# Performance work log

Hardware: AMD Instinct MI355X
Metric: run time of the kernel (lower is better)

Reference implementation:

```python
import jax, jax.numpy as jnp
import numpy as np

EPS = 1e-5


def _gcn_norm(edge_index, N):
    # symmetric GCN normalization with self-loops: D^-1/2 (A+I) D^-1/2
    row, col = edge_index[0], edge_index[1]
    loop = jnp.arange(N, dtype=row.dtype)
    row_f = jnp.concatenate([row, loop])
    col_f = jnp.concatenate([col, loop])
    deg = jax.ops.segment_sum(jnp.ones_like(row_f, dtype=jnp.float32), row_f, num_segments=N)
    dinv = jnp.where(deg > 0, jax.lax.rsqrt(jnp.maximum(deg, 1.0)), 0.0)
    norm = dinv[row_f] * dinv[col_f]  # [E+N]
    return row_f, col_f, norm


def _gcn_conv(h, W, b, row_f, col_f, norm, N):
    h = h @ W  # [N, C_out] small GEMM
    msg = h[col_f] * norm[:, None]  # gather over edges  [E+N, C_out]
    return jax.ops.segment_sum(msg, row_f, num_segments=N) + b


def _bn_eval(h, gamma, beta, mean, var):
    return (h - mean) * jax.lax.rsqrt(var + EPS) * gamma + beta


def setup_inputs() -> dict:
    key = jax.random.key(0)
    ks = jax.random.split(key, 12)
    N, E = 100000, 1600000
    C_in, C_hid, C_out = 64, 64, 64
    x = jax.random.normal(ks[0], (N, C_in), dtype=jnp.float32)
    edge_index = jax.random.randint(ks[1], (2, E), 0, N, dtype=jnp.int32)
    s = 1.0 / np.sqrt(C_hid)
    inp = {
        "x": x,
        "edge_index": edge_index,
        "W1": jax.random.normal(ks[2], (C_in, C_hid), dtype=jnp.float32) * s,
        "b1": jnp.zeros((C_hid,), jnp.float32),
        "g1": jnp.ones((C_hid,), jnp.float32),
        "be1": jnp.zeros((C_hid,), jnp.float32),
        "m1": jax.random.normal(ks[3], (C_hid,), dtype=jnp.float32) * 0.1,
        "v1": jax.random.uniform(ks[4], (C_hid,), minval=0.5, maxval=1.5, dtype=jnp.float32),
        "W2": jax.random.normal(ks[5], (C_hid, C_hid), dtype=jnp.float32) * s,
        "b2": jnp.zeros((C_hid,), jnp.float32),
        "g2": jnp.ones((C_hid,), jnp.float32),
        "be2": jnp.zeros((C_hid,), jnp.float32),
        "m2": jax.random.normal(ks[6], (C_hid,), dtype=jnp.float32) * 0.1,
        "v2": jax.random.uniform(ks[7], (C_hid,), minval=0.5, maxval=1.5, dtype=jnp.float32),
        "W3": jax.random.normal(ks[8], (C_hid, C_out), dtype=jnp.float32) * s,
        "b3": jnp.zeros((C_out,), jnp.float32),
    }
    return inp


def reference(x, edge_index, W1, b1, g1, be1, m1, v1, W2, b2, g2, be2, m2, v2, W3, b3):
    N = x.shape[0]
    row_f, col_f, norm = _gcn_norm(edge_index, N)  # cached=True: computed once
    h = _gcn_conv(x, W1, b1, row_f, col_f, norm, N)
    h = jax.nn.relu(_bn_eval(h, g1, be1, m1, v1))  # dropout off (eval)
    h = _gcn_conv(h, W2, b2, row_f, col_f, norm, N)
    h = jax.nn.relu(_bn_eval(h, g2, be2, m2, v2))
    global_embeddings = h
    hc_predictions = _gcn_conv(global_embeddings, W3, b3, row_f, col_f, norm, N)
    return (global_embeddings, hc_predictions)
```

## Files before the change

### kernel.cpp

```cpp
#include <hip/hip_runtime.h>

typedef __attribute__((ext_vector_type(8))) short bfrag8;
typedef __attribute__((ext_vector_type(4))) float facc4;
typedef __attribute__((ext_vector_type(8))) unsigned short u16x8;

#define CROWS  256
#define NCBMAX 512
#define CAP    8192
#define CHUNK  4096
#define SLACK  772
#define BPITCH (CAP + SLACK)

static __device__ __forceinline__ float bf2f(ushort u) {
    union { unsigned int i; float f; } x;
    x.i = ((unsigned int)u) << 16;
    return x.f;
}
static __device__ __forceinline__ ushort f2bf(float f) {
    union { float f; unsigned int i; } x;
    x.f = f;
    unsigned int r = x.i + 0x7FFFu + ((x.i >> 16) & 1u);
    return (ushort)(r >> 16);
}

__global__ void k_prep(const float* __restrict__ W1, const float* __restrict__ W2,
                       const float* __restrict__ W3,
                       const float* __restrict__ b1, const float* __restrict__ g1,
                       const float* __restrict__ be1, const float* __restrict__ m1,
                       const float* __restrict__ v1,
                       const float* __restrict__ b2, const float* __restrict__ g2,
                       const float* __restrict__ be2, const float* __restrict__ m2,
                       const float* __restrict__ v2,
                       const float* __restrict__ b3,
                       ushort* __restrict__ wp, float* __restrict__ pp,
                       int* __restrict__ ccur, int ncb,
                       ushort* __restrict__ ta, ushort* __restrict__ tb, int N) {
    int l = blockIdx.x;
    if (l < 3) {
        const float* W = (l == 0) ? W1 : (l == 1) ? W2 : W3;
        ushort* wo = wp + l * 4096;
        for (int idx = threadIdx.x; idx < 4096; idx += blockDim.x) {
            int j = idx & 7, m = (idx >> 3) & 15, quad = (idx >> 7) & 3;
            int ks = (idx >> 9) & 1, c2 = idx >> 10;
            wo[idx] = f2bf(W[(32 * ks + 8 * quad + j) * 64 + c2 * 16 + m]);
        }
        if (threadIdx.x < 64) {
            int ch = threadIdx.x;
            float PS, PH;
            if (l == 0) {
                float sc = g1[ch] * rsqrtf(v1[ch] + 1e-5f);
                PS = sc; PH = be1[ch] - m1[ch] * sc + b1[ch] * sc;
            } else if (l == 1) {
                float sc = g2[ch] * rsqrtf(v2[ch] + 1e-5f);
                PS = sc; PH = be2[ch] - m2[ch] * sc + b2[ch] * sc;
            } else {
                PS = 1.f; PH = b3[ch];
            }
            pp[l * 128 + ch] = PS;
            pp[l * 128 + 64 + ch] = PH;
        }
    } else {
        for (int b = threadIdx.x; b < ncb; b += blockDim.x) ccur[b] = b * CAP;
        if (threadIdx.x < 128) {
            int t = threadIdx.x;
            if (t < 64) ta[(size_t)N * 64 + t] = 0;
            else        tb[(size_t)N * 64 + (t - 64)] = 0;
        }
    }
}

__global__ void k_part(const int* __restrict__ row, const int* __restrict__ col, int E,
                       int* __restrict__ ccur, int* __restrict__ bkt, int ncb) {
    __shared__ int recs[CHUNK];
    __shared__ unsigned short cbl[CHUNK];
    __shared__ int recs2[CHUNK];
    __shared__ int gofs[CHUNK];
    __shared__ int hist[NCBMAX], lbase[NCBMAX], loff[NCBMAX], lpos[NCBMAX];
    int tid = threadIdx.x;
    int chunk0 = blockIdx.x * CHUNK;
    int cnt = min(CHUNK, E - chunk0);

    for (int i = tid; i < NCBMAX; i += blockDim.x) { hist[i] = 0; }
    __syncthreads();
    for (int j = tid; j < cnt; j += blockDim.x) {
        int r = row[chunk0 + j];
        int cb = r >> 8;
        recs[j] = ((r & (CROWS - 1)) << 17) | col[chunk0 + j];
        cbl[j] = (unsigned short)cb;
        atomicAdd(&hist[cb], 1);
    }
    __syncthreads();
    for (int i = tid; i < ncb; i += blockDim.x) {
        int h = hist[i];
        lbase[i] = h ? atomicAdd(&ccur[i], h) : 0;
        loff[i] = 0;
    }
    if (tid < NCBMAX) lpos[tid] = hist[tid];
    __syncthreads();
    #pragma unroll
    for (int off = 1; off < NCBMAX; off <<= 1) {
        int t = (tid < NCBMAX && tid >= off) ? lpos[tid - off] : 0;
        __syncthreads();
        if (tid < NCBMAX) lpos[tid] += t;
        __syncthreads();
    }
    for (int j = tid; j < cnt; j += blockDim.x) {
        int cb = cbl[j];
        int p = atomicAdd(&loff[cb], 1);
        int lp = lpos[cb] - hist[cb] + p;
        recs2[lp] = recs[j];
        int gp = lbase[cb] + p;
        gofs[lp] = (gp < (cb + 1) * CAP) ? gp : -1;
    }
    __syncthreads();
    for (int t = tid; t < cnt; t += blockDim.x) {
        int g = gofs[t];
        if (g >= 0) bkt[g] = recs2[t];
    }
}

__global__ void k_build(const int* __restrict__ bkt, const int* __restrict__ ccur,
                        int* __restrict__ rptr, int* __restrict__ deg,
                        float* __restrict__ dinv, int* __restrict__ cidx, int N) {
    __shared__ int hist[CROWS], wstart[CROWS], cur[CROWS], psum[CROWS];
    int tid = threadIdx.x;
    int b = blockIdx.x;
    int lo = b * CROWS;
    int nr = min(CROWS, N - lo);
    int in0 = b * CAP;
    int cntE = min(ccur[b] - in0, CAP);
    int out0 = b * BPITCH;

    if (tid < CROWS) hist[tid] = 0;
    __syncthreads();
    for (int i = tid; i < cntE; i += blockDim.x)
        atomicAdd(&hist[bkt[in0 + i] >> 17], 1);
    __syncthreads();
    int d = 0, ep = 0;
    if (tid < CROWS) {
        d = hist[tid];
        ep = (d + 3) & ~3;
        psum[tid] = ep;
    }
    __syncthreads();
    #pragma unroll
    for (int off = 1; off < CROWS; off <<= 1) {
        int t = (tid >= off && tid < CROWS) ? psum[tid - off] : 0;
        __syncthreads();
        if (tid < CROWS) psum[tid] += t;
        __syncthreads();
    }
    if (tid < CROWS) {
        int ws = out0 + psum[tid] - ep;
        wstart[tid] = ws;
        cur[tid] = ws;
        if (tid < nr) {
            rptr[lo + tid] = ws;
            deg[lo + tid] = d;
            dinv[lo + tid] = rsqrtf((float)(d + 1));
        }
    }
    __syncthreads();
    for (int i = tid; i < cntE; i += blockDim.x) {
        int v = bkt[in0 + i];
        int p = atomicAdd(&cur[v >> 17], 1);
        cidx[p] = v & 0x1FFFF;
    }
    __syncthreads();
    if (tid < nr) {
        int dd = hist[tid];
        int epp = (dd + 3) & ~3;
        for (int j = dd; j < epp; j++) cidx[wstart[tid] + j] = N;
    }
}

__global__ void k_gemm(const float* __restrict__ Hv, const ushort* __restrict__ wq,
                       const float* __restrict__ dinv,
                       ushort* __restrict__ T, int ntiles, int N) {
    int lane = threadIdx.x & 63;
    int wid = (blockIdx.x * blockDim.x + threadIdx.x) >> 6;
    int nw = (gridDim.x * blockDim.x) >> 6;
    int m = lane & 15, quad = lane >> 4;

    bfrag8 bf[2][4];
    #pragma unroll
    for (int s = 0; s < 2; s++)
        #pragma unroll
        for (int c = 0; c < 4; c++)
            bf[s][c] = *(const bfrag8*)(wq +
                (size_t)((((c * 2 + s) * 4 + quad) * 16 + m) * 8));

    for (int t = wid; t < ntiles; t += nw) {
        int nodeA = t * 16 + m;
        if (nodeA >= N) nodeA = N - 1;
        bfrag8 a0, a1;
        const float* arow = Hv + (size_t)nodeA * 64;
        #pragma unroll
        for (int s = 0; s < 2; s++) {
            float4 u0 = *(const float4*)(arow + s * 32 + quad * 8);
            float4 u1 = *(const float4*)(arow + s * 32 + quad * 8 + 4);
            bfrag8 f;
            f[0] = (short)f2bf(u0.x); f[1] = (short)f2bf(u0.y);
            f[2] = (short)f2bf(u0.z); f[3] = (short)f2bf(u0.w);
            f[4] = (short)f2bf(u1.x); f[5] = (short)f2bf(u1.y);
            f[6] = (short)f2bf(u1.z); f[7] = (short)f2bf(u1.w);
            if (s == 0) a0 = f; else a1 = f;
        }
        facc4 acc[4];
        #pragma unroll
        for (int c = 0; c < 4; c++) { acc[c][0]=0.f; acc[c][1]=0.f; acc[c][2]=0.f; acc[c][3]=0.f; }
        #pragma unroll
        for (int c = 0; c < 4; c++) {
            acc[c] = __builtin_amdgcn_mfma_f32_16x16x32_bf16(a0, bf[0][c], acc[c], 0, 0, 0);
            acc[c] = __builtin_amdgcn_mfma_f32_16x16x32_bf16(a1, bf[1][c], acc[c], 0, 0, 0);
        }
        #pragma unroll
        for (int c = 0; c < 4; c++)
            #pragma unroll
            for (int r = 0; r < 4; r++) {
                int node = t * 16 + quad * 4 + r;
                if (node < N)
                    T[(size_t)node * 64 + c * 16 + m] = f2bf(dinv[node] * acc[c][r]);
            }
    }
}

template <bool FUSE>
__global__ void __launch_bounds__(256, 6)
k_aggf(const ushort* __restrict__ T2, const int* __restrict__ rptr,
       const int* __restrict__ deg, const float* __restrict__ dinv,
       const int* __restrict__ cidx,
       const float* __restrict__ pp, int relu,
       const ushort* __restrict__ wq,
       float* __restrict__ outf, ushort* __restrict__ Tn, int N) {
    __shared__ ushort lds_h[32][72];

    int tid = threadIdx.x;
    int lane = tid & 63;
    int wl = tid >> 6;
    int grp = lane >> 3;
    int s = lane & 7;
    int loc = wl * 8 + grp;
    int r = blockIdx.x * 32 + loc;
    bool rv = (r < N);
    int rs = rv ? r : N;

    int start = rv ? rptr[r] : 0;
    int ep = rv ? ((deg[r] + 3) & ~3) : 0;
    u16x8 sf = *(const u16x8*)(T2 + (size_t)rs * 64 + s * 8);
    float dr = rv ? dinv[r] : 0.f;

    float a[8];
    #pragma unroll
    for (int k = 0; k < 8; k++) a[k] = 0.f;

    int i = 0;
    bool have8 = (8 <= ep);
    int4 c4, d4;
    if (have8) {
        c4 = *(const int4*)(cidx + start);
        d4 = *(const int4*)(cidx + start + 4);
    }
    while (have8) {
        int ni = i + 8;
        bool nhave = (ni + 8 <= ep);
        int4 nc4, nd4;
        if (nhave) {
            nc4 = *(const int4*)(cidx + start + ni);
            nd4 = *(const int4*)(cidx + start + ni + 4);
        }
        u16x8 t0 = *(const u16x8*)(T2 + (size_t)c4.x * 64 + s * 8);
        u16x8 t1 = *(const u16x8*)(T2 + (size_t)c4.y * 64 + s * 8);
        u16x8 t2 = *(const u16x8*)(T2 + (size_t)c4.z * 64 + s * 8);
        u16x8 t3 = *(const u16x8*)(T2 + (size_t)c4.w * 64 + s * 8);
        u16x8 t4 = *(const u16x8*)(T2 + (size_t)d4.x * 64 + s * 8);
        u16x8 t5 = *(const u16x8*)(T2 + (size_t)d4.y * 64 + s * 8);
        u16x8 t6 = *(const u16x8*)(T2 + (size_t)d4.z * 64 + s * 8);
        u16x8 t7 = *(const u16x8*)(T2 + (size_t)d4.w * 64 + s * 8);
        #pragma unroll
        for (int k = 0; k < 8; k++)
            a[k] += ((bf2f(t0[k]) + bf2f(t1[k])) + (bf2f(t2[k]) + bf2f(t3[k]))) +
                    ((bf2f(t4[k]) + bf2f(t5[k])) + (bf2f(t6[k]) + bf2f(t7[k])));
        c4 = nc4; d4 = nd4; i = ni; have8 = nhave;
    }
    if (i < ep) {
        int4 e4 = *(const int4*)(cidx + start + i);
        u16x8 t0 = *(const u16x8*)(T2 + (size_t)e4.x * 64 + s * 8);
        u16x8 t1 = *(const u16x8*)(T2 + (size_t)e4.y * 64 + s * 8);
        u16x8 t2 = *(const u16x8*)(T2 + (size_t)e4.z * 64 + s * 8);
        u16x8 t3 = *(const u16x8*)(T2 + (size_t)e4.w * 64 + s * 8);
        #pragma unroll
        for (int k = 0; k < 8; k++)
            a[k] += (bf2f(t0[k]) + bf2f(t1[k])) + (bf2f(t2[k]) + bf2f(t3[k]));
    }

    float4 ps0 = *(const float4*)(pp + s * 8);
    float4 ps1 = *(const float4*)(pp + s * 8 + 4);
    float4 ph0 = *(const float4*)(pp + 64 + s * 8);
    float4 ph1 = *(const float4*)(pp + 64 + s * 8 + 4);
    float PS[8] = {ps0.x, ps0.y, ps0.z, ps0.w, ps1.x, ps1.y, ps1.z, ps1.w};
    float PH[8] = {ph0.x, ph0.y, ph0.z, ph0.w, ph1.x, ph1.y, ph1.z, ph1.w};

    float v[8];
    #pragma unroll
    for (int k = 0; k < 8; k++) v[k] = 0.f;
    if (rv) {
        #pragma unroll
        for (int k = 0; k < 8; k++) {
            v[k] = dr * (a[k] + bf2f(sf[k])) * PS[k] + PH[k];
            if (relu) v[k] = fmaxf(v[k], 0.f);
        }
        if (outf) {
            *(float4*)(outf + (size_t)r * 64 + s * 8) = make_float4(v[0], v[1], v[2], v[3]);
            *(float4*)(outf + (size_t)r * 64 + s * 8 + 4) = make_float4(v[4], v[5], v[6], v[7]);
        }
    }

    if constexpr (FUSE) {
        u16x8 hv;
        #pragma unroll
        for (int k = 0; k < 8; k++) hv[k] = rv ? f2bf(v[k]) : (ushort)0;
        *(u16x8*)&lds_h[loc][s * 8] = hv;

        int m = lane & 15, quad = lane >> 4;
        int rtile = wl >> 1, chalf = wl & 1;
        bfrag8 bw[2][2];
        #pragma unroll
        for (int ks = 0; ks < 2; ks++)
            #pragma unroll
            for (int c = 0; c < 2; c++)
                bw[ks][c] = *(const bfrag8*)(wq +
                    (size_t)(((((chalf * 2 + c) * 2 + ks) * 4 + quad) * 16 + m) * 8));
        __syncthreads();

        bfrag8 a0 = *(const bfrag8*)&lds_h[rtile * 16 + m][quad * 8];
        bfrag8 a1 = *(const bfrag8*)&lds_h[rtile * 16 + m][32 + quad * 8];
        facc4 acc[2];
        #pragma unroll
        for (int c = 0; c < 2; c++) { acc[c][0]=0.f; acc[c][1]=0.f; acc[c][2]=0.f; acc[c][3]=0.f; }
        #pragma unroll
        for (int c = 0; c < 2; c++) {
            acc[c] = __builtin_amdgcn_mfma_f32_16x16x32_bf16(a0, bw[0][c], acc[c], 0, 0, 0);
            acc[c] = __builtin_amdgcn_mfma_f32_16x16x32_bf16(a1, bw[1][c], acc[c], 0, 0, 0);
        }
        int nodeBase = blockIdx.x * 32 + rtile * 16;
        #pragma unroll
        for (int c = 0; c < 2; c++)
            #pragma unroll
            for (int rr = 0; rr < 4; rr++) {
                int node = nodeBase + quad * 4 + rr;
                if (node < N)
                    Tn[(size_t)node * 64 + (chalf * 2 + c) * 16 + m] =
                        f2bf(dinv[node] * acc[c][rr]);
            }
    }
}


extern "C" void kernel_launch(void* const* d_in, const int* in_sizes, int n_in,
                              void* d_out, int out_size, void* d_ws, size_t ws_size,
                              hipStream_t stream) {
    const float* x  = (const float*)d_in[0];
    const int*   ei = (const int*)d_in[1];
    const float *W1 = (const float*)d_in[2],  *b1 = (const float*)d_in[3];
    const float *g1 = (const float*)d_in[4],  *be1= (const float*)d_in[5];
    const float *m1 = (const float*)d_in[6],  *v1 = (const float*)d_in[7];
    const float *W2 = (const float*)d_in[8],  *b2 = (const float*)d_in[9];
    const float *g2 = (const float*)d_in[10], *be2= (const float*)d_in[11];
    const float *m2 = (const float*)d_in[12], *v2 = (const float*)d_in[13];
    const float *W3 = (const float*)d_in[14], *b3 = (const float*)d_in[15];

    int N = in_sizes[0] / 64;
    int E = in_sizes[1] / 2;
    const int* row = ei;
    const int* col = ei + E;
    int ncb = (N + CROWS - 1) / CROWS;

    char* p = (char*)d_ws;
    auto take = [&](size_t b) -> char* {
        char* q = p;
        p += (b + 255) & ~(size_t)255;
        return q;
    };
    int*    ccur  = (int*)   take((size_t)ncb * 4);
    int*    rptr  = (int*)   take((size_t)N * 4);
    int*    deg   = (int*)   take((size_t)N * 4);
    float*  dinv  = (float*) take((size_t)N * 4);
    ushort* wp    = (ushort*)take((size_t)3 * 4096 * 2);
    float*  pp    = (float*) take((size_t)3 * 128 * 4);
    int*    bkt   = (int*)   take((size_t)ncb * CAP * 4);
    int*    cidx  = (int*)   take((size_t)ncb * BPITCH * 4 + 1024);
    ushort* ta    = (ushort*)take((size_t)(N + 1) * 64 * 2);
    ushort* tb    = (ushort*)take((size_t)(N + 1) * 64 * 2);

    const int TB = 256;
    const int TBP = 1024;
    int nchunks = (E + CHUNK - 1) / CHUNK;
    k_prep <<<4, TB, 0, stream>>>(W1, W2, W3, b1, g1, be1, m1, v1,
                                  b2, g2, be2, m2, v2, b3, wp, pp,
                                  ccur, ncb, ta, tb, N);
    k_part <<<nchunks, TBP, 0, stream>>>(row, col, E, ccur, bkt, ncb);
    k_build<<<ncb, TBP, 0, stream>>>(bkt, ccur, rptr, deg, dinv, cidx, N);

    float* outp = (float*)d_out;
    int ntiles = (N + 15) >> 4;
    int GG = (ntiles + 3) / 4;
    int GA = (N + 31) / 32;

    k_gemm<<<GG, TB, 0, stream>>>(x, wp, dinv, ta, ntiles, N);
    k_aggf<true><<<GA, TB, 0, stream>>>(ta, rptr, deg, dinv, cidx, pp, 1,
                                        wp + 4096, (float*)nullptr, tb, N);
    k_aggf<true><<<GA, TB, 0, stream>>>(tb, rptr, deg, dinv, cidx, pp + 128, 1,
                                        wp + 8192, outp, ta, N);
    k_aggf<false><<<GA, TB, 0, stream>>>(ta, rptr, deg, dinv, cidx, pp + 256, 0,
                                         (const ushort*)nullptr,
                                         outp + (size_t)N * 64, (ushort*)nullptr, N);
}
```

Measured before the change: 255.0 us.

## Count degrees in partition pass, widen aggregation unroll to 16 edges

Degree counting moves from a shared-memory histogram pass in k_build to global atomics in k_part, which needs an extra memset of deg. This removes one full read of the bucket array in k_build but adds many scattered global atomics. The aggregation loop now issues 16 neighbour gathers per iteration instead of 8 with software-prefetched indices. Its launch bound is relaxed from 6 to 4 blocks per CU, giving more registers per thread at the cost of occupancy.

```diff
diff --git a/kernel.cpp b/kernel.cpp
--- a/kernel.cpp
+++ b/kernel.cpp
@@ -69,8 +69,9 @@
     }
 }
 
-__global__ void k_part(const int* __restrict__ row, const int* __restrict__ col, int E,
-                       int* __restrict__ ccur, int* __restrict__ bkt, int ncb) {
+__global__ void __launch_bounds__(1024)
+k_part(const int* __restrict__ row, const int* __restrict__ col, int E,
+       int* __restrict__ ccur, int* __restrict__ bkt, int* __restrict__ deg, int ncb) {
     __shared__ int recs[CHUNK];
     __shared__ unsigned short cbl[CHUNK];
     __shared__ int recs2[CHUNK];
@@ -80,7 +81,7 @@
     int chunk0 = blockIdx.x * CHUNK;
     int cnt = min(CHUNK, E - chunk0);
 
-    for (int i = tid; i < NCBMAX; i += blockDim.x) { hist[i] = 0; }
+    for (int i = tid; i < NCBMAX; i += blockDim.x) hist[i] = 0;
     __syncthreads();
     for (int j = tid; j < cnt; j += blockDim.x) {
         int r = row[chunk0 + j];
@@ -88,6 +89,7 @@
         recs[j] = ((r & (CROWS - 1)) << 17) | col[chunk0 + j];
         cbl[j] = (unsigned short)cb;
         atomicAdd(&hist[cb], 1);
+        atomicAdd(&deg[r], 1);
     }
     __syncthreads();
     for (int i = tid; i < ncb; i += blockDim.x) {
@@ -119,10 +121,12 @@
     }
 }
 
-__global__ void k_build(const int* __restrict__ bkt, const int* __restrict__ ccur,
-                        int* __restrict__ rptr, int* __restrict__ deg,
-                        float* __restrict__ dinv, int* __restrict__ cidx, int N) {
-    __shared__ int hist[CROWS], wstart[CROWS], cur[CROWS], psum[CROWS];
+__global__ void __launch_bounds__(1024)
+k_build(const int* __restrict__ bkt, const int* __restrict__ ccur,
+        const int* __restrict__ deg,
+        int* __restrict__ rptr, float* __restrict__ dinv,
+        int* __restrict__ cidx, int N) {
+    __shared__ int wstart[CROWS], cur[CROWS], psum[CROWS];
     int tid = threadIdx.x;
     int b = blockIdx.x;
     int lo = b * CROWS;
@@ -131,14 +135,9 @@
     int cntE = min(ccur[b] - in0, CAP);
     int out0 = b * BPITCH;
 
-    if (tid < CROWS) hist[tid] = 0;
-    __syncthreads();
-    for (int i = tid; i < cntE; i += blockDim.x)
-        atomicAdd(&hist[bkt[in0 + i] >> 17], 1);
-    __syncthreads();
     int d = 0, ep = 0;
     if (tid < CROWS) {
-        d = hist[tid];
+        d = (tid < nr) ? deg[lo + tid] : 0;
         ep = (d + 3) & ~3;
         psum[tid] = ep;
     }
@@ -156,7 +155,6 @@
         cur[tid] = ws;
         if (tid < nr) {
             rptr[lo + tid] = ws;
-            deg[lo + tid] = d;
             dinv[lo + tid] = rsqrtf((float)(d + 1));
         }
     }
@@ -167,11 +165,8 @@
         cidx[p] = v & 0x1FFFF;
     }
     __syncthreads();
-    if (tid < nr) {
-        int dd = hist[tid];
-        int epp = (dd + 3) & ~3;
-        for (int j = dd; j < epp; j++) cidx[wstart[tid] + j] = N;
-    }
+    if (tid < nr)
+        for (int j = d; j < ep; j++) cidx[wstart[tid] + j] = N;
 }
 
 __global__ void k_gemm(const float* __restrict__ Hv, const ushort* __restrict__ wq,
@@ -226,7 +221,7 @@
 }
 
 template <bool FUSE>
-__global__ void __launch_bounds__(256, 6)
+__global__ void __launch_bounds__(256, 4)
 k_aggf(const ushort* __restrict__ T2, const int* __restrict__ rptr,
        const int* __restrict__ deg, const float* __restrict__ dinv,
        const int* __restrict__ cidx,
@@ -255,35 +250,35 @@
     for (int k = 0; k < 8; k++) a[k] = 0.f;
 
     int i = 0;
-    bool have8 = (8 <= ep);
-    int4 c4, d4;
-    if (have8) {
-        c4 = *(const int4*)(cidx + start);
-        d4 = *(const int4*)(cidx + start + 4);
-    }
-    while (have8) {
-        int ni = i + 8;
-        bool nhave = (ni + 8 <= ep);
-        int4 nc4, nd4;
-        if (nhave) {
-            nc4 = *(const int4*)(cidx + start + ni);
-            nd4 = *(const int4*)(cidx + start + ni + 4);
-        }
-        u16x8 t0 = *(const u16x8*)(T2 + (size_t)c4.x * 64 + s * 8);
-        u16x8 t1 = *(const u16x8*)(T2 + (size_t)c4.y * 64 + s * 8);
-        u16x8 t2 = *(const u16x8*)(T2 + (size_t)c4.z * 64 + s * 8);
-        u16x8 t3 = *(const u16x8*)(T2 + (size_t)c4.w * 64 + s * 8);
-        u16x8 t4 = *(const u16x8*)(T2 + (size_t)d4.x * 64 + s * 8);
-        u16x8 t5 = *(const u16x8*)(T2 + (size_t)d4.y * 64 + s * 8);
-        u16x8 t6 = *(const u16x8*)(T2 + (size_t)d4.z * 64 + s * 8);
-        u16x8 t7 = *(const u16x8*)(T2 + (size_t)d4.w * 64 + s * 8);
+    for (; i + 16 <= ep; i += 16) {
+        int4 a0 = *(const int4*)(cidx + start + i);
+        int4 a1 = *(const int4*)(cidx + start + i + 4);
+        int4 b0 = *(const int4*)(cidx + start + i + 8);
+        int4 b1 = *(const int4*)(cidx + start + i + 12);
+        u16x8 t0 = *(const u16x8*)(T2 + (size_t)a0.x * 64 + s * 8);
+        u16x8 t1 = *(const u16x8*)(T2 + (size_t)a0.y * 64 + s * 8);
+        u16x8 t2 = *(const u16x8*)(T2 + (size_t)a0.z * 64 + s * 8);
+        u16x8 t3 = *(const u16x8*)(T2 + (size_t)a0.w * 64 + s * 8);
+        u16x8 t4 = *(const u16x8*)(T2 + (size_t)a1.x * 64 + s * 8);
+        u16x8 t5 = *(const u16x8*)(T2 + (size_t)a1.y * 64 + s * 8);
+        u16x8 t6 = *(const u16x8*)(T2 + (size_t)a1.z * 64 + s * 8);
+        u16x8 t7 = *(const u16x8*)(T2 + (size_t)a1.w * 64 + s * 8);
+        u16x8 u0 = *(const u16x8*)(T2 + (size_t)b0.x * 64 + s * 8);
+        u16x8 u1 = *(const u16x8*)(T2 + (size_t)b0.y * 64 + s * 8);
+        u16x8 u2 = *(const u16x8*)(T2 + (size_t)b0.z * 64 + s * 8);
+        u16x8 u3 = *(const u16x8*)(T2 + (size_t)b0.w * 64 + s * 8);
+        u16x8 u4 = *(const u16x8*)(T2 + (size_t)b1.x * 64 + s * 8);
+        u16x8 u5 = *(const u16x8*)(T2 + (size_t)b1.y * 64 + s * 8);
+        u16x8 u6 = *(const u16x8*)(T2 + (size_t)b1.z * 64 + s * 8);
+        u16x8 u7 = *(const u16x8*)(T2 + (size_t)b1.w * 64 + s * 8);
         #pragma unroll
         for (int k = 0; k < 8; k++)
-            a[k] += ((bf2f(t0[k]) + bf2f(t1[k])) + (bf2f(t2[k]) + bf2f(t3[k]))) +
-                    ((bf2f(t4[k]) + bf2f(t5[k])) + (bf2f(t6[k]) + bf2f(t7[k])));
-        c4 = nc4; d4 = nd4; i = ni; have8 = nhave;
-    }
-    if (i < ep) {
+            a[k] += (((bf2f(t0[k]) + bf2f(t1[k])) + (bf2f(t2[k]) + bf2f(t3[k]))) +
+                     ((bf2f(t4[k]) + bf2f(t5[k])) + (bf2f(t6[k]) + bf2f(t7[k])))) +
+                    (((bf2f(u0[k]) + bf2f(u1[k])) + (bf2f(u2[k]) + bf2f(u3[k]))) +
+                     ((bf2f(u4[k]) + bf2f(u5[k])) + (bf2f(u6[k]) + bf2f(u7[k]))));
+    }
+    for (; i < ep; i += 4) {
         int4 e4 = *(const int4*)(cidx + start + i);
         u16x8 t0 = *(const u16x8*)(T2 + (size_t)e4.x * 64 + s * 8);
         u16x8 t1 = *(const u16x8*)(T2 + (size_t)e4.y * 64 + s * 8);
@@ -394,13 +389,14 @@
     ushort* tb    = (ushort*)take((size_t)(N + 1) * 64 * 2);
 
     const int TB = 256;
-    const int TBP = 1024;
     int nchunks = (E + CHUNK - 1) / CHUNK;
+
+    hipMemsetAsync(deg, 0, (size_t)N * 4, stream);
     k_prep <<<4, TB, 0, stream>>>(W1, W2, W3, b1, g1, be1, m1, v1,
                                   b2, g2, be2, m2, v2, b3, wp, pp,
                                   ccur, ncb, ta, tb, N);
-    k_part <<<nchunks, TBP, 0, stream>>>(row, col, E, ccur, bkt, ncb);
-    k_build<<<ncb, TBP, 0, stream>>>(bkt, ccur, rptr, deg, dinv, cidx, N);
+    k_part <<<nchunks, 1024, 0, stream>>>(row, col, E, ccur, bkt, deg, ncb);
+    k_build<<<ncb, 1024, 0, stream>>>(bkt, ccur, deg, rptr, dinv, cidx, N);
 
     float* outp = (float*)d_out;
     int ntiles = (N + 15) >> 4;
```

After: 323.6 us. 1.27x slower.
